# Performance work log

Measured on AMD Instinct MI355X. Metric: run time of the kernel, lower is better.

Reference implementation:

```python
import jax, jax.numpy as jnp
import numpy as np
import math

INPUT_SIZE = 1024
HIDDEN_SIZE = 1024
BATCH = 4096


def setup_inputs() -> dict:
    key = jax.random.key(0)
    ks = jax.random.split(key, 16)
    stddev = 1.0 / math.sqrt(HIDDEN_SIZE)

    def unif(k, shape):
        return jax.random.uniform(k, shape, minval=-stddev, maxval=stddev, dtype=jnp.float32)

    inp = {
        'x': jax.random.normal(ks[0], (BATCH, INPUT_SIZE), dtype=jnp.float32),
        'h_prev': jax.random.normal(ks[1], (BATCH, HIDDEN_SIZE), dtype=jnp.float32),
        'c_prev': jax.random.normal(ks[2], (BATCH, HIDDEN_SIZE), dtype=jnp.float32),
        'igx': unif(ks[3], (INPUT_SIZE, HIDDEN_SIZE)),
        'igu': unif(ks[4], (HIDDEN_SIZE, HIDDEN_SIZE)),
        'ib': unif(ks[5], (HIDDEN_SIZE,)),
        'fgx': unif(ks[6], (INPUT_SIZE, HIDDEN_SIZE)),
        'fgu': unif(ks[7], (HIDDEN_SIZE, HIDDEN_SIZE)),
        'fb': unif(ks[8], (HIDDEN_SIZE,)),
        'ogx': unif(ks[9], (INPUT_SIZE, HIDDEN_SIZE)),
        'ogu': unif(ks[10], (HIDDEN_SIZE, HIDDEN_SIZE)),
        'ob': unif(ks[11], (HIDDEN_SIZE,)),
        'cgx': unif(ks[12], (INPUT_SIZE, HIDDEN_SIZE)),
        'cgu': unif(ks[13], (HIDDEN_SIZE, HIDDEN_SIZE)),
        'cb': unif(ks[14], (HIDDEN_SIZE,)),
    }
    return inp


def reference(x, h_prev, c_prev, igx, igu, ib, fgx, fgu, fb, ogx, ogu, ob, cgx, cgu, cb):
    # Fuse the 8 gate matmuls into 2 GEMMs via concatenated weights.
    # Wx: [input_size, 4H], Wh: [hidden, 4H], b: [4H]; gate order i,f,o,c.
    Wx = jnp.concatenate([igx, fgx, ogx, cgx], axis=1)
    Wh = jnp.concatenate([igu, fgu, ogu, cgu], axis=1)
    b = jnp.concatenate([ib, fb, ob, cb], axis=0)
    gates = x @ Wx + h_prev @ Wh + b  # [B, 4H]
    H = c_prev.shape[-1]
    ig = jax.nn.sigmoid(gates[:, 0 * H:1 * H])
    fg = jax.nn.sigmoid(gates[:, 1 * H:2 * H])
    og = jax.nn.sigmoid(gates[:, 2 * H:3 * H])
    cc = jnp.tanh(gates[:, 3 * H:4 * H])
    c = fg * c_prev + ig * cc
    h = og * jnp.tanh(c)
    return (h, c)
```

## Files before the change

### kernel.cpp

```cpp
#include <hip/hip_runtime.h>
#include <hip/hip_bf16.h>

typedef unsigned short u16;
typedef unsigned int u32;
typedef short bf16x8 __attribute__((ext_vector_type(8)));
typedef float f32x4 __attribute__((ext_vector_type(4)));
typedef u16 u16x8 __attribute__((ext_vector_type(8)));

#define HID 1024
#define BATCH 4096
#define KTOT 2048

__device__ __forceinline__ u16 f2bf(float f) {
  u32 v = __builtin_bit_cast(u32, f);
  u32 r = (v + 0x7fffu + ((v >> 16) & 1u)) >> 16;
  return (u16)r;
}
__device__ __forceinline__ float sigmoid_fast(float x) {
  return 1.0f / (1.0f + __expf(-x));
}
__device__ __forceinline__ float tanh_fast(float x) {
  return 2.0f * sigmoid_fast(2.0f * x) - 1.0f;
}
__device__ __forceinline__ void gl_lds16(const void* g, void* l) {
  __builtin_amdgcn_global_load_lds(
      (const __attribute__((address_space(1))) u32*)g,
      (__attribute__((address_space(3))) u32*)l, 16, 0, 0);
}

__global__ __launch_bounds__(256) void prep_xh(
    const float* __restrict__ x, const float* __restrict__ hp,
    u16* __restrict__ xh) {
  int c = blockIdx.x * 256 + threadIdx.x;
  int row = c >> 8;
  int col0 = (c & 255) << 3;
  const float* src = (col0 < 1024) ? (x + (size_t)row * 1024 + col0)
                                   : (hp + (size_t)row * 1024 + (col0 - 1024));
  f32x4 a = *(const f32x4*)(src);
  f32x4 b = *(const f32x4*)(src + 4);
  u16x8 v;
#pragma unroll
  for (int j = 0; j < 4; ++j) { v[j] = f2bf(a[j]); v[j + 4] = f2bf(b[j]); }
  *(u16x8*)(xh + (size_t)row * KTOT + col0) = v;
}

__global__ __launch_bounds__(256) void prep_w(
    const float* __restrict__ igx, const float* __restrict__ fgx,
    const float* __restrict__ ogx, const float* __restrict__ cgx,
    const float* __restrict__ igu, const float* __restrict__ fgu,
    const float* __restrict__ ogu, const float* __restrict__ cgu,
    u16* __restrict__ bt) {
  __shared__ u16 lds[64 * 66];
  const float* srcs[8] = {igx, fgx, ogx, cgx, igu, fgu, ogu, cgu};
  int bid = blockIdx.x;
  int m = bid >> 8;
  int tile = bid & 255;
  int th = tile & 15, tk = tile >> 4;
  int h0 = th << 6, k0 = tk << 6;
  int g = m & 3, which = m >> 2;
  const float* W = srcs[m] + (size_t)k0 * HID + h0;

  int t = threadIdx.x;

  int r1 = t >> 4;
  int c1 = (t & 15) << 2;
#pragma unroll
  for (int p = 0; p < 4; ++p) {
    int row = (p << 4) + r1;
    f32x4 v = *(const f32x4*)(W + (size_t)row * HID + c1);
    u32 p0 = (u32)f2bf(v[0]) | ((u32)f2bf(v[1]) << 16);
    u32 p1 = (u32)f2bf(v[2]) | ((u32)f2bf(v[3]) << 16);
    u32* d = (u32*)&lds[row * 66 + c1];
    d[0] = p0;
    d[1] = p1;
  }
  __syncthreads();

  int nl = t >> 2;
  int kc = t & 3;
  int row_np = ((h0 >> 4) << 6) + ((nl >> 4) << 6) + (g << 4) + (nl & 15);
  size_t dst = (size_t)row_np * KTOT + (size_t)which * 1024 + k0;
  u16x8 a, b;
#pragma unroll
  for (int j = 0; j < 8; ++j) {
    a[j] = lds[(kc * 8 + j) * 66 + nl];
    b[j] = lds[(kc * 8 + 32 + j) * 66 + nl];
  }
  *(u16x8*)(&bt[dst + kc * 8]) = a;
  *(u16x8*)(&bt[dst + kc * 8 + 32]) = b;
}

__global__ __launch_bounds__(256) void lstm_gemm(
    const u16* __restrict__ xh, const u16* __restrict__ bt,
    const float* __restrict__ cprev,
    const float* __restrict__ ib, const float* __restrict__ fb,
    const float* __restrict__ ob, const float* __restrict__ cb,
    float* __restrict__ hout, float* __restrict__ cout) {
  __shared__ u16 As[128 * 32];
  __shared__ u16 Bs[128 * 32];

  int t = threadIdx.x;
  int brow = blockIdx.x, bcol = blockIdx.y;
  int w = t >> 6, l = t & 63;
  int wr = (w >> 1) * 64, wc = (w & 1) * 64;
  int lrow = l & 15, quad = l >> 4;

  f32x4 acc[4][4] = {};

  int srow = t >> 2;
  int schunk = ((t & 3) ^ ((t >> 3) & 3)) << 3;
  int quadp = ((quad ^ ((lrow >> 1) & 3)) << 3);
  int grow = brow * 128;
  size_t brow_b = (size_t)(bcol * 128);

  for (int kt = 0; kt < 64; ++kt) {
    __syncthreads();
    int kk = kt * 32;
    gl_lds16(xh + (size_t)(grow + srow) * KTOT + kk + schunk, &As[t * 8]);
    gl_lds16(xh + (size_t)(grow + srow + 64) * KTOT + kk + schunk, &As[(t + 256) * 8]);
    gl_lds16(bt + (brow_b + srow) * KTOT + kk + schunk, &Bs[t * 8]);
    gl_lds16(bt + (brow_b + srow + 64) * KTOT + kk + schunk, &Bs[(t + 256) * 8]);
    __syncthreads();

    bf16x8 af[4], bfr[4];
#pragma unroll
    for (int i = 0; i < 4; ++i) {
      af[i]  = *(const bf16x8*)&As[(wr + i * 16 + lrow) * 32 + quadp];
      bfr[i] = *(const bf16x8*)&Bs[(wc + i * 16 + lrow) * 32 + quadp];
    }
#pragma unroll
    for (int mi = 0; mi < 4; ++mi)
#pragma unroll
      for (int ni = 0; ni < 4; ++ni)
        acc[mi][ni] = __builtin_amdgcn_mfma_f32_16x16x32_bf16(
            af[mi], bfr[ni], acc[mi][ni], 0, 0, 0);
  }

  int sb = bcol * 2 + (w & 1);
  int hcol = sb * 16 + lrow;
  float bi = ib[hcol];
  float bff = fb[hcol];
  float bo = ob[hcol];
  float bc = cb[hcol];

#pragma unroll
  for (int mi = 0; mi < 4; ++mi) {
    int row0 = grow + wr + mi * 16 + quad * 4;
#pragma unroll
    for (int r = 0; r < 4; ++r) {
      size_t idx = (size_t)(row0 + r) * HID + hcol;
      float gi = sigmoid_fast(acc[mi][0][r] + bi);
      float gf = sigmoid_fast(acc[mi][1][r] + bff);
      float go = sigmoid_fast(acc[mi][2][r] + bo);
      float gc = tanh_fast(acc[mi][3][r] + bc);
      float cp = cprev[idx];
      float cv = gf * cp + gi * gc;
      float hv = go * tanh_fast(cv);
      hout[idx] = hv;
      cout[idx] = cv;
    }
  }
}

extern "C" void kernel_launch(void* const* d_in, const int* in_sizes, int n_in,
                              void* d_out, int out_size, void* d_ws, size_t ws_size,
                              hipStream_t stream) {
  const float* x   = (const float*)d_in[0];
  const float* hp  = (const float*)d_in[1];
  const float* cp  = (const float*)d_in[2];
  const float* igx = (const float*)d_in[3];
  const float* igu = (const float*)d_in[4];
  const float* ib  = (const float*)d_in[5];
  const float* fgx = (const float*)d_in[6];
  const float* fgu = (const float*)d_in[7];
  const float* fb  = (const float*)d_in[8];
  const float* ogx = (const float*)d_in[9];
  const float* ogu = (const float*)d_in[10];
  const float* ob  = (const float*)d_in[11];
  const float* cgx = (const float*)d_in[12];
  const float* cgu = (const float*)d_in[13];
  const float* cb  = (const float*)d_in[14];

  u16* bt = (u16*)d_ws;
  u16* xh = bt + (size_t)4096 * 2048;
  float* hout = (float*)d_out;
  float* cout = hout + (size_t)BATCH * HID;

  prep_xh<<<4096, 256, 0, stream>>>(x, hp, xh);
  prep_w<<<2048, 256, 0, stream>>>(igx, fgx, ogx, cgx, igu, fgu, ogu, cgu, bt);
  lstm_gemm<<<dim3(32, 32), 256, 0, stream>>>(xh, bt, cp, ib, fb, ob, cb,
                                              hout, cout);
}
```

Baseline: 234.6 us.

## Pre-pack operands into MFMA fragment layout and load directly from global

Prep kernels now write x/h and weights in per-lane MFMA fragment order, 512 elements per 16x32 tile. The GEMM drops LDS staging and barriers and has each wave load its bf16x8 fragments straight from global memory, with launch bounds requesting higher occupancy. The aim is to remove LDS traffic and synchronisation. The cost is duplicated global/L2 reads, since operands are no longer shared across waves through LDS, and there is no explicit prefetch to hide load latency.

```diff
diff --git a/kernel.cpp b/kernel.cpp
--- a/kernel.cpp
+++ b/kernel.cpp
@@ -22,26 +22,24 @@
 __device__ __forceinline__ float tanh_fast(float x) {
   return 2.0f * sigmoid_fast(2.0f * x) - 1.0f;
 }
-__device__ __forceinline__ void gl_lds16(const void* g, void* l) {
-  __builtin_amdgcn_global_load_lds(
-      (const __attribute__((address_space(1))) u32*)g,
-      (__attribute__((address_space(3))) u32*)l, 16, 0, 0);
-}
 
 __global__ __launch_bounds__(256) void prep_xh(
     const float* __restrict__ x, const float* __restrict__ hp,
-    u16* __restrict__ xh) {
-  int c = blockIdx.x * 256 + threadIdx.x;
-  int row = c >> 8;
-  int col0 = (c & 255) << 3;
-  const float* src = (col0 < 1024) ? (x + (size_t)row * 1024 + col0)
-                                   : (hp + (size_t)row * 1024 + (col0 - 1024));
+    u16* __restrict__ xh2) {
+  int s = blockIdx.x * 256 + threadIdx.x;
+  int lane = s & 63, unit = s >> 6;
+  int kstep = unit & 63, rowtile = unit >> 6;
+  int m = lane & 15, quad = lane >> 4;
+  int row = rowtile * 16 + m;
+  int kg = kstep * 32 + quad * 8;
+  const float* src = (kg < 1024) ? (x + (size_t)row * 1024 + kg)
+                                 : (hp + (size_t)row * 1024 + (kg - 1024));
   f32x4 a = *(const f32x4*)(src);
   f32x4 b = *(const f32x4*)(src + 4);
   u16x8 v;
 #pragma unroll
   for (int j = 0; j < 4; ++j) { v[j] = f2bf(a[j]); v[j + 4] = f2bf(b[j]); }
-  *(u16x8*)(xh + (size_t)row * KTOT + col0) = v;
+  *(u16x8*)(xh2 + (size_t)s * 8) = v;
 }
 
 __global__ __launch_bounds__(256) void prep_w(
@@ -78,55 +76,44 @@
 
   int nl = t >> 2;
   int kc = t & 3;
-  int row_np = ((h0 >> 4) << 6) + ((nl >> 4) << 6) + (g << 4) + (nl & 15);
-  size_t dst = (size_t)row_np * KTOT + (size_t)which * 1024 + k0;
+  int np = (((h0 + nl) >> 4) << 6) + (g << 4) + ((h0 + nl) & 15);
+  int ntile = np >> 4, m16 = np & 15;
+  int kstep = which * 32 + (k0 >> 5);
+  size_t unit = (size_t)ntile * 64 + kstep;
+  int lane16 = kc * 16 + m16;
   u16x8 a, b;
 #pragma unroll
   for (int j = 0; j < 8; ++j) {
     a[j] = lds[(kc * 8 + j) * 66 + nl];
     b[j] = lds[(kc * 8 + 32 + j) * 66 + nl];
   }
-  *(u16x8*)(&bt[dst + kc * 8]) = a;
-  *(u16x8*)(&bt[dst + kc * 8 + 32]) = b;
+  *(u16x8*)(&bt[unit * 512 + lane16 * 8]) = a;
+  *(u16x8*)(&bt[(unit + 1) * 512 + lane16 * 8]) = b;
 }
 
-__global__ __launch_bounds__(256) void lstm_gemm(
-    const u16* __restrict__ xh, const u16* __restrict__ bt,
+__global__ __launch_bounds__(256, 4) void lstm_gemm(
+    const u16* __restrict__ xh2, const u16* __restrict__ bt,
     const float* __restrict__ cprev,
     const float* __restrict__ ib, const float* __restrict__ fb,
     const float* __restrict__ ob, const float* __restrict__ cb,
     float* __restrict__ hout, float* __restrict__ cout) {
-  __shared__ u16 As[128 * 32];
-  __shared__ u16 Bs[128 * 32];
-
   int t = threadIdx.x;
   int brow = blockIdx.x, bcol = blockIdx.y;
   int w = t >> 6, l = t & 63;
-  int wr = (w >> 1) * 64, wc = (w & 1) * 64;
+  int wr = (w >> 1) * 64;
   int lrow = l & 15, quad = l >> 4;
 
   f32x4 acc[4][4] = {};
 
-  int srow = t >> 2;
-  int schunk = ((t & 3) ^ ((t >> 3) & 3)) << 3;
-  int quadp = ((quad ^ ((lrow >> 1) & 3)) << 3);
-  int grow = brow * 128;
-  size_t brow_b = (size_t)(bcol * 128);
+  const u16* pA = xh2 + ((size_t)(brow * 8 + (w >> 1) * 4) * 64) * 512 + l * 8;
+  const u16* pB = bt  + ((size_t)(bcol * 8 + (w & 1) * 4) * 64) * 512 + l * 8;
 
   for (int kt = 0; kt < 64; ++kt) {
-    __syncthreads();
-    int kk = kt * 32;
-    gl_lds16(xh + (size_t)(grow + srow) * KTOT + kk + schunk, &As[t * 8]);
-    gl_lds16(xh + (size_t)(grow + srow + 64) * KTOT + kk + schunk, &As[(t + 256) * 8]);
-    gl_lds16(bt + (brow_b + srow) * KTOT + kk + schunk, &Bs[t * 8]);
-    gl_lds16(bt + (brow_b + srow + 64) * KTOT + kk + schunk, &Bs[(t + 256) * 8]);
-    __syncthreads();
-
     bf16x8 af[4], bfr[4];
 #pragma unroll
     for (int i = 0; i < 4; ++i) {
-      af[i]  = *(const bf16x8*)&As[(wr + i * 16 + lrow) * 32 + quadp];
-      bfr[i] = *(const bf16x8*)&Bs[(wc + i * 16 + lrow) * 32 + quadp];
+      af[i]  = *(const bf16x8*)(pA + (size_t)(i * 64 + kt) * 512);
+      bfr[i] = *(const bf16x8*)(pB + (size_t)(i * 64 + kt) * 512);
     }
 #pragma unroll
     for (int mi = 0; mi < 4; ++mi)
@@ -142,6 +129,7 @@
   float bff = fb[hcol];
   float bo = ob[hcol];
   float bc = cb[hcol];
+  int grow = brow * 128;
 
 #pragma unroll
   for (int mi = 0; mi < 4; ++mi) {
@@ -181,13 +169,13 @@
   const float* cgu = (const float*)d_in[13];
   const float* cb  = (const float*)d_in[14];
 
-  u16* bt = (u16*)d_ws;
-  u16* xh = bt + (size_t)4096 * 2048;
+  u16* bt  = (u16*)d_ws;
+  u16* xh2 = bt + (size_t)4096 * 2048;
   float* hout = (float*)d_out;
   float* cout = hout + (size_t)BATCH * HID;
 
-  prep_xh<<<4096, 256, 0, stream>>>(x, hp, xh);
+  prep_xh<<<4096, 256, 0, stream>>>(x, hp, xh2);
   prep_w<<<2048, 256, 0, stream>>>(igx, fgx, ogx, cgx, igu, fgu, ogu, cgu, bt);
-  lstm_gemm<<<dim3(32, 32), 256, 0, stream>>>(xh, bt, cp, ib, fb, ob, cb,
+  lstm_gemm<<<dim3(32, 32), 256, 0, stream>>>(xh2, bt, cp, ib, fb, ob, cb,
                                               hout, cout);
 }
```

After: 235.6 us. Within noise of the previous version (+0.5%).
